# Performance work log

Hardware: AMD Instinct MI355X
Metric: run time of the kernel (lower is better)

The kernel has to match this reference:

```python
import jax, jax.numpy as jnp
import numpy as np

B, S, D = 4, 4096, 1024
H = 16
DH = D // H  # 64, required by the fused kernel


def setup_inputs() -> dict:
    key = jax.random.key(0)
    ks = jax.random.split(key, 5)
    scale = 1.0 / np.sqrt(D)  # xavier-ish init scale for square matrices
    return {
        "x": jax.random.normal(ks[0], (B, S, D), dtype=jnp.float32),
        "Wq": jax.random.normal(ks[1], (D, D), dtype=jnp.float32) * scale,
        "Wk": jax.random.normal(ks[2], (D, D), dtype=jnp.float32) * scale,
        "Wv": jax.random.normal(ks[3], (D, D), dtype=jnp.float32) * scale,
        "Wo": jax.random.normal(ks[4], (D, D), dtype=jnp.float32) * scale,
    }


def reference(x, Wq, Wk, Wv, Wo):
    # Fused QKV projection + linear (non-softmax) attention.
    # Q = x Wq, K = x Wk, V = x Wv, split into H heads of size DH.
    b, s, d = x.shape
    h, dh = H, d // H

    def to_heads(t):
        return t.reshape(b, s, h, dh).transpose(0, 2, 1, 3)  # [B,H,S,dh]

    q = to_heads(jnp.einsum("bsd,de->bse", x, Wq))
    k = to_heads(jnp.einsum("bsd,de->bse", x, Wk))
    v = to_heads(jnp.einsum("bsd,de->bse", x, Wv))

    # Linear attention: O(S * dh^2) per head, never materializes [S,S].
    # out = (1/sqrt(dh)) * Q @ (K^T V)
    scale = 1.0 / jnp.sqrt(jnp.asarray(dh, dtype=x.dtype))
    kv = jnp.einsum("bhsd,bhse->bhde", k, v)          # [B,H,dh,dh]
    out = jnp.einsum("bhsd,bhde->bhse", q, kv) * scale  # [B,H,S,dh]

    # kernel output [B,H,S,dh] -> transpose(1,2) -> view [B,S,D]
    out = out.transpose(0, 2, 1, 3).reshape(b, s, d)
    # out_proj: nn.Linear(D, D, bias=False) -> x @ W.T
    return jnp.einsum("bsd,ed->bse", out, Wo)
```

## Files before the change

### kernel.cpp

```cpp
#include <hip/hip_runtime.h>

typedef unsigned short u16;
typedef unsigned int u32;
typedef u16 u16x8 __attribute__((ext_vector_type(8)));
typedef u16 u16x4 __attribute__((ext_vector_type(4)));
typedef __bf16 bf16x8 __attribute__((ext_vector_type(8)));
typedef float f32x4 __attribute__((ext_vector_type(4)));

__device__ __forceinline__ u16 f2bf(float f) {
    u32 u = __builtin_bit_cast(u32, f);
    u32 r = (u + 0x7fffu + ((u >> 16) & 1u)) >> 16;
    return (u16)r;
}
__device__ __forceinline__ void async16(const u16* g, u16* lds_base) {
    __builtin_amdgcn_global_load_lds(
        (const __attribute__((address_space(1))) void*)g,
        (__attribute__((address_space(3))) void*)lds_base, 16, 0, 0);
}
__device__ __forceinline__ void storeC(float* p, float v) { *p = v; }
__device__ __forceinline__ void storeC(u16* p, float v)   { *p = f2bf(v); }

__global__ void cvt_f32_bf16(const float* __restrict__ in, u16* __restrict__ out, long n) {
    long idx = ((long)blockIdx.x * blockDim.x + threadIdx.x) * 8;
    if (idx >= n) return;
    float4 a = *(const float4*)(in + idx);
    float4 b = *(const float4*)(in + idx + 4);
    u16x8 o;
    o[0] = f2bf(a.x); o[1] = f2bf(a.y); o[2] = f2bf(a.z); o[3] = f2bf(a.w);
    o[4] = f2bf(b.x); o[5] = f2bf(b.y); o[6] = f2bf(b.z); o[7] = f2bf(b.w);
    *(u16x8*)(out + idx) = o;
}

__global__ void transpose_cvt(const float* __restrict__ W0, const float* __restrict__ W1,
                              const float* __restrict__ W2, u16* __restrict__ WT) {
    __shared__ float tile[32][33];
    const float* W = (blockIdx.z == 0) ? W0 : (blockIdx.z == 1) ? W1 : W2;
    int n0 = blockIdx.x * 32, k0 = blockIdx.y * 32;
    int tx = threadIdx.x, ty = threadIdx.y;
#pragma unroll
    for (int r = 0; r < 4; ++r)
        tile[ty + 8 * r][tx] = W[(size_t)(k0 + ty + 8 * r) * 1024 + n0 + tx];
    __syncthreads();
#pragma unroll
    for (int r = 0; r < 4; ++r) {
        int n = n0 + ty + 8 * r;
        WT[((size_t)blockIdx.z * 1024 + n) * 1024 + k0 + tx] = f2bf(tile[tx][ty + 8 * r]);
    }
}

#define BAR __builtin_amdgcn_s_barrier()
#define WAITLGK do { asm volatile("s_waitcnt lgkmcnt(0)" ::: "memory"); \
                     __builtin_amdgcn_sched_barrier(0); } while (0)
#define PRIO1 __builtin_amdgcn_s_setprio(1)
#define PRIO0 __builtin_amdgcn_s_setprio(0)
#define VM(n) asm volatile("s_waitcnt vmcnt(" #n ")" ::: "memory")

#define As SM[0]
#define Bs SM[1]

#define LDA(buf, mh) do { _Pragma("unroll") for (int mi = 0; mi < 4; ++mi) { \
    const int rA = (wm * 128 + (mh) * 64 + mi * 16 + frow) * 64; \
    aF[mi][0] = *(const bf16x8*)&As[buf][rA + xs0]; \
    aF[mi][1] = *(const bf16x8*)&As[buf][rA + xs1]; } } while (0)

#define LDB(buf, nh) do { _Pragma("unroll") for (int ni = 0; ni < 2; ++ni) { \
    const int rB = (wn * 64 + (nh) * 32 + ni * 16 + frow) * 64; \
    bF[(nh) * 2 + ni][0] = *(const bf16x8*)&Bs[buf][rB + xs0]; \
    bF[(nh) * 2 + ni][1] = *(const bf16x8*)&Bs[buf][rB + xs1]; } } while (0)

#define MFQ(mh, nh) do { _Pragma("unroll") for (int mi = 0; mi < 4; ++mi) \
  _Pragma("unroll") for (int ni = 0; ni < 2; ++ni) \
  _Pragma("unroll") for (int s = 0; s < 2; ++s) \
    acc[(mh) * 4 + mi][(nh) * 2 + ni] = __builtin_amdgcn_mfma_f32_16x16x32_bf16( \
        aF[mi][s], bF[(nh) * 2 + ni][s], acc[(mh) * 4 + mi][(nh) * 2 + ni], 0, 0, 0); } while (0)

#define TILE4(buf, S1, S2, S3, S4, WV) \
  LDA(buf, 0); LDB(buf, 0); S1; BAR; WAITLGK; PRIO1; MFQ(0, 0); PRIO0; BAR; \
  LDB(buf, 1); S2; BAR; WAITLGK; PRIO1; MFQ(0, 1); PRIO0; BAR; \
  LDA(buf, 1); S3; BAR; WAITLGK; PRIO1; MFQ(1, 1); PRIO0; BAR; \
  S4; BAR; WAITLGK; PRIO1; MFQ(1, 0); PRIO0; WV; BAR;

template <typename OutT, bool QKV>
__global__ __launch_bounds__(512, 2) void gemm8p(
    const u16* __restrict__ A, int lda,
    const u16* __restrict__ Bt, int ldb,
    OutT* __restrict__ Cq, int ldc, int K, int nTN,
    size_t btStrideB, u16* __restrict__ Kt, u16* __restrict__ Vt) {
    __shared__ u16 SM[2][2][256 * 64];
    const int tid = threadIdx.x;
    const int wid = tid >> 6, lane = tid & 63;
    const int wm = wid >> 2, wn = wid & 3;

    const int nwg = gridDim.x;
    const int orig = blockIdx.x;
    const int id = (orig & 7) * (nwg >> 3) + (orig >> 3);
    const size_t mBase = (size_t)(id / nTN) * 256;
    const size_t nBase = (size_t)(id % nTN) * 256;

    if (!QKV) Bt += (mBase >> 12) * btStrideB;

    const int srow = lane >> 3;
    const int scol = (((lane & 7) ^ (srow & 7)) * 8);

    auto stageH = [&](int buf, int isB, int h, int kt) {
        const u16* g = isB ? Bt : A;
        const int ld = isB ? ldb : lda;
        const size_t rb = isB ? nBase : mBase;
        u16* lds = isB ? Bs[buf] : As[buf];
#pragma unroll
        for (int j = 0; j < 2; ++j) {
            const int rowL = isB ? ((wid >> 1) * 64 + h * 32 + (wid & 1) * 16 + j * 8)
                                 : ((wid >> 2) * 128 + h * 64 + (wid & 3) * 16 + j * 8);
            async16(g + (rb + rowL + srow) * (size_t)ld + (size_t)kt * 64 + scol,
                    lds + rowL * 64);
        }
    };

    const int frow = lane & 15;
    const int xs0 = (((lane >> 4)) ^ (frow & 7)) * 8;
    const int xs1 = ((4 + (lane >> 4)) ^ (frow & 7)) * 8;

    f32x4 acc[8][4] = {};
    bf16x8 aF[4][2], bF[4][2];

#pragma unroll
    for (int h = 0; h < 2; ++h) { stageH(0, 0, h, 0); stageH(0, 1, h, 0); }
#pragma unroll
    for (int h = 0; h < 2; ++h) { stageH(1, 0, h, 1); stageH(1, 1, h, 1); }
    VM(8);
    BAR;

    const int np = K >> 7;
    for (int p = 0; p < np - 1; ++p) {
        const int k2 = 2 * p + 2, k3 = 2 * p + 3;
        TILE4(0, ,
              { stageH(0, 0, 0, k2); stageH(0, 1, 0, k2); },
              stageH(0, 1, 1, k2),
              stageH(0, 0, 1, k2),
              VM(8));
        TILE4(1, ,
              { stageH(1, 0, 0, k3); stageH(1, 1, 0, k3); },
              stageH(1, 1, 1, k3),
              stageH(1, 0, 1, k3),
              VM(8));
    }
    TILE4(0, , , , , VM(0));
    TILE4(1, , , , , );

    const int rb4 = (lane >> 4) * 4;
    const int cx = lane & 15;
    const int sel = QKV ? (int)(nBase >> 10) : 0;
    if (!QKV || sel == 0) {
#pragma unroll
        for (int m = 0; m < 8; ++m) {
#pragma unroll
            for (int n = 0; n < 4; ++n) {
                const size_t col = nBase + wn * 64 + n * 16 + cx;
#pragma unroll
                for (int r = 0; r < 4; ++r) {
                    const size_t row = mBase + wm * 128 + m * 16 + rb4 + r;
                    storeC(&Cq[row * (size_t)ldc + col], acc[m][n][r]);
                }
            }
        }
    } else {
        __syncthreads();
        u16* T = &SM[0][0][0];
        const int nLoc = (int)(nBase & 1023);
#pragma unroll
        for (int n = 0; n < 4; ++n) {
            const int colL = wn * 64 + n * 16 + cx;
#pragma unroll
            for (int m = 0; m < 8; ++m) {
                const int R = wm * 128 + m * 16 + rb4;
                u16x4 v;
                v[0] = f2bf(acc[m][n][0]); v[1] = f2bf(acc[m][n][1]);
                v[2] = f2bf(acc[m][n][2]); v[3] = f2bf(acc[m][n][3]);
                const int byteoff = colL * 512 + ((((R >> 3) ^ (colL & 31)) << 4) | ((R & 7) << 1));
                *(u16x4*)((char*)T + byteoff) = v;
            }
        }
        __syncthreads();
        const int b = (int)(mBase >> 12);
        u16* KV = (sel == 1 ? Kt : Vt);
        const int j = lane & 31;
#pragma unroll
        for (int u = 0; u < 16; ++u) {
            const int iLoc = wid * 32 + u * 2 + (lane >> 5);
            const int byteoff = iLoc * 512 + ((j ^ (iLoc & 31)) << 4);
            const int gcol = nLoc + iLoc;
            u16* dst = KV + (((size_t)(b * 16 + (gcol >> 6)) * 64 + (gcol & 63)) << 12)
                          + (mBase & 4095) + j * 8;
            *(u16x8*)dst = *(const u16x8*)((char*)T + byteoff);
        }
    }
}

__global__ __launch_bounds__(256, 2) void kv_gemm(
    const u16* __restrict__ Kt, const u16* __restrict__ Vt, float* __restrict__ P) {
    __shared__ u16 Ks[64 * 64];
    __shared__ u16 Vs[64 * 64];
    const int chunk = blockIdx.x, bh = blockIdx.y;
    const int tid = threadIdx.x, w = tid >> 6, lane = tid & 63;
    const int srow = lane >> 3;
    const int scol = ((lane & 7) ^ srow) * 8;
    const int frow = lane & 15;
    const int xs0 = ((lane >> 4) ^ (frow & 7)) * 8;
    const int xs1 = ((4 + (lane >> 4)) ^ (frow & 7)) * 8;
    const size_t base = (size_t)bh * 64 * 4096 + (size_t)chunk * 512;
    f32x4 acc[4] = {};
    for (int kk = 0; kk < 8; ++kk) {
        __syncthreads();
#pragma unroll
        for (int j = 0; j < 2; ++j) {
            const int row = w * 16 + j * 8;
            async16(Kt + base + (size_t)(row + srow) * 4096 + kk * 64 + scol, &Ks[row * 64]);
            async16(Vt + base + (size_t)(row + srow) * 4096 + kk * 64 + scol, &Vs[row * 64]);
        }
        asm volatile("s_waitcnt vmcnt(0)" ::: "memory");
        __syncthreads();
        bf16x8 a0 = *(const bf16x8*)&Ks[(w * 16 + frow) * 64 + xs0];
        bf16x8 a1 = *(const bf16x8*)&Ks[(w * 16 + frow) * 64 + xs1];
#pragma unroll
        for (int n = 0; n < 4; ++n) {
            bf16x8 b0 = *(const bf16x8*)&Vs[(n * 16 + frow) * 64 + xs0];
            bf16x8 b1 = *(const bf16x8*)&Vs[(n * 16 + frow) * 64 + xs1];
            acc[n] = __builtin_amdgcn_mfma_f32_16x16x32_bf16(a0, b0, acc[n], 0, 0, 0);
            acc[n] = __builtin_amdgcn_mfma_f32_16x16x32_bf16(a1, b1, acc[n], 0, 0, 0);
        }
    }
    const int rb4 = (lane >> 4) * 4, cx = lane & 15;
    float* p = P + ((size_t)chunk * 64 + bh) * 4096;
#pragma unroll
    for (int n = 0; n < 4; ++n)
#pragma unroll
        for (int r = 0; r < 4; ++r)
            p[(w * 16 + rb4 + r) * 64 + n * 16 + cx] = acc[n][r];
}

__global__ void kv_reduce(const float* __restrict__ P, u16* __restrict__ kvb) {
    const int bh = blockIdx.x, t = threadIdx.x;
    for (int idx = t; idx < 4096; idx += 256) {
        float s = 0.f;
#pragma unroll
        for (int c = 0; c < 8; ++c) s += P[((size_t)c * 64 + bh) * 4096 + idx];
        kvb[(size_t)bh * 4096 + idx] = f2bf(s * 0.125f);
    }
}

__global__ __launch_bounds__(256, 2) void w2_gemm(
    const u16* __restrict__ Wob, const u16* __restrict__ kvb, u16* __restrict__ W2t) {
    __shared__ u16 Aw[256 * 64];
    __shared__ u16 Bw[64 * 64];
    const int eT = blockIdx.x, h = blockIdx.y, b = blockIdx.z;
    const int tid = threadIdx.x, w = tid >> 6, lane = tid & 63;
    const int srow = lane >> 3;
    const int scol = ((lane & 7) ^ srow) * 8;
#pragma unroll
    for (int j = 0; j < 8; ++j) {
        const int row = w * 64 + j * 8;
        async16(Wob + (size_t)(eT * 256 + row + srow) * 1024 + h * 64 + scol, &Aw[row * 64]);
    }
#pragma unroll
    for (int j = 0; j < 2; ++j) {
        const int row = w * 16 + j * 8;
        async16(kvb + ((size_t)(b * 16 + h) * 64 + row + srow) * 64 + scol, &Bw[row * 64]);
    }
    asm volatile("s_waitcnt vmcnt(0)" ::: "memory");
    __syncthreads();
    const int frow = lane & 15;
    const int xs0 = ((lane >> 4) ^ (frow & 7)) * 8;
    const int xs1 = ((4 + (lane >> 4)) ^ (frow & 7)) * 8;
    f32x4 acc[4][4] = {};
#pragma unroll
    for (int m = 0; m < 4; ++m) {
        bf16x8 a0 = *(const bf16x8*)&Aw[(w * 64 + m * 16 + frow) * 64 + xs0];
        bf16x8 a1 = *(const bf16x8*)&Aw[(w * 64 + m * 16 + frow) * 64 + xs1];
#pragma unroll
        for (int n = 0; n < 4; ++n) {
            bf16x8 b0 = *(const bf16x8*)&Bw[(n * 16 + frow) * 64 + xs0];
            bf16x8 b1 = *(const bf16x8*)&Bw[(n * 16 + frow) * 64 + xs1];
            acc[m][n] = __builtin_amdgcn_mfma_f32_16x16x32_bf16(a0, b0, acc[m][n], 0, 0, 0);
            acc[m][n] = __builtin_amdgcn_mfma_f32_16x16x32_bf16(a1, b1, acc[m][n], 0, 0, 0);
        }
    }
    const int rb4 = (lane >> 4) * 4, cx = lane & 15;
    u16* out = W2t + (size_t)b * 1048576;
#pragma unroll
    for (int m = 0; m < 4; ++m)
#pragma unroll
        for (int n = 0; n < 4; ++n)
#pragma unroll
            for (int r = 0; r < 4; ++r)
                out[(size_t)(eT * 256 + w * 64 + m * 16 + rb4 + r) * 1024 + h * 64 + n * 16 + cx] =
                    f2bf(acc[m][n][r]);
}

extern "C" void kernel_launch(void* const* d_in, const int* in_sizes, int n_in,
                              void* d_out, int out_size, void* d_ws, size_t ws_size,
                              hipStream_t stream) {
    const float* x  = (const float*)d_in[0];
    const float* Wq = (const float*)d_in[1];
    const float* Wk = (const float*)d_in[2];
    const float* Wv = (const float*)d_in[3];
    const float* Wo = (const float*)d_in[4];
    float* out = (float*)d_out;
    char* ws = (char*)d_ws;

    u16*   Yq    = (u16*)(ws);
    u16*   Kt    = (u16*)(ws + 33554432);
    u16*   Vt    = (u16*)(ws + 67108864);
    u16*   xb    = (u16*)(ws + 100663296);
    float* Pkv   = (float*)(ws + 100663296);
    u16*   kvb   = (u16*)(ws + 109051904);
    u16*   W2t   = (u16*)(ws + 109576192);
    u16*   WqkvT = (u16*)(ws + 134217728);
    u16*   Wob   = (u16*)(ws + 140509184);

    cvt_f32_bf16<<<8192, 256, 0, stream>>>(x, xb, 16777216L);
    cvt_f32_bf16<<<512, 256, 0, stream>>>(Wo, Wob, 1048576L);
    transpose_cvt<<<dim3(32, 32, 3), dim3(32, 8), 0, stream>>>(Wq, Wk, Wv, WqkvT);

    gemm8p<u16, true><<<768, 512, 0, stream>>>(xb, 1024, WqkvT, 1024, Yq, 1024, 1024, 12,
                                               0, Kt, Vt);

    kv_gemm<<<dim3(8, 64), 256, 0, stream>>>(Kt, Vt, Pkv);
    kv_reduce<<<64, 256, 0, stream>>>(Pkv, kvb);
    w2_gemm<<<dim3(4, 16, 4), 256, 0, stream>>>(Wob, kvb, W2t);

    gemm8p<float, false><<<256, 512, 0, stream>>>(Yq, 1024, W2t, 1024, out, 1024, 1024, 4,
                                                  1048576, nullptr, nullptr);
}
```

Before: 188.2 us.

## Fold Wq into per-batch output weight to skip the Q projection GEMM

```diff
diff --git a/kernel.cpp b/kernel.cpp
--- a/kernel.cpp
+++ b/kernel.cpp
@@ -32,9 +32,9 @@
 }
 
 __global__ void transpose_cvt(const float* __restrict__ W0, const float* __restrict__ W1,
-                              const float* __restrict__ W2, u16* __restrict__ WT) {
+                              u16* __restrict__ WT) {
     __shared__ float tile[32][33];
-    const float* W = (blockIdx.z == 0) ? W0 : (blockIdx.z == 1) ? W1 : W2;
+    const float* W = (blockIdx.z == 0) ? W0 : W1;
     int n0 = blockIdx.x * 32, k0 = blockIdx.y * 32;
     int tx = threadIdx.x, ty = threadIdx.y;
 #pragma unroll
@@ -80,7 +80,7 @@
   LDA(buf, 1); S3; BAR; WAITLGK; PRIO1; MFQ(1, 1); PRIO0; BAR; \
   S4; BAR; WAITLGK; PRIO1; MFQ(1, 0); PRIO0; WV; BAR;
 
-template <typename OutT, bool QKV>
+template <typename OutT, bool KVMODE>
 __global__ __launch_bounds__(512, 2) void gemm8p(
     const u16* __restrict__ A, int lda,
     const u16* __restrict__ Bt, int ldb,
@@ -97,7 +97,7 @@
     const size_t mBase = (size_t)(id / nTN) * 256;
     const size_t nBase = (size_t)(id % nTN) * 256;
 
-    if (!QKV) Bt += (mBase >> 12) * btStrideB;
+    if (!KVMODE) Bt += (mBase >> 12) * btStrideB;
 
     const int srow = lane >> 3;
     const int scol = (((lane & 7) ^ (srow & 7)) * 8);
@@ -149,8 +149,7 @@
 
     const int rb4 = (lane >> 4) * 4;
     const int cx = lane & 15;
-    const int sel = QKV ? (int)(nBase >> 10) : 0;
-    if (!QKV || sel == 0) {
+    if (!KVMODE) {
 #pragma unroll
         for (int m = 0; m < 8; ++m) {
 #pragma unroll
@@ -182,7 +181,7 @@
         }
         __syncthreads();
         const int b = (int)(mBase >> 12);
-        u16* KV = (sel == 1 ? Kt : Vt);
+        u16* KV = ((nBase >> 10) == 0 ? Kt : Vt);
         const int j = lane & 31;
 #pragma unroll
         for (int u = 0; u < 16; ++u) {
@@ -194,6 +193,78 @@
             *(u16x8*)dst = *(const u16x8*)((char*)T + byteoff);
         }
     }
+}
+
+__global__ __launch_bounds__(256, 2) void gemm128(
+    const u16* __restrict__ A, int lda,
+    const u16* __restrict__ Bt, int ldb,
+    u16* __restrict__ C, int ldc, int K) {
+    __shared__ u16 A2[2][128 * 64];
+    __shared__ u16 B2[2][128 * 64];
+    const int tid = threadIdx.x, w = tid >> 6, lane = tid & 63;
+    const int wr = w >> 1, wc = w & 1;
+    const size_t mBase = (size_t)blockIdx.y * 128;
+    const size_t nBase = (size_t)blockIdx.x * 128;
+    const int lr = lane >> 3;
+    const int scol = ((lane & 7) ^ lr) * 8;
+
+    auto stage = [&](int buf, int kt) {
+#pragma unroll
+        for (int c = 0; c < 2; ++c) {
+            const u16* g = c ? Bt : A;
+            const int ld = c ? ldb : lda;
+            const size_t rb = c ? nBase : mBase;
+            u16* lds = c ? B2[buf] : A2[buf];
+#pragma unroll
+            for (int jj = 0; jj < 4; ++jj) {
+                const int rowL = jj * 32 + w * 8;
+                async16(g + (rb + rowL + lr) * (size_t)ld + (size_t)kt * 64 + scol,
+                        lds + rowL * 64);
+            }
+        }
+    };
+
+    const int frow = lane & 15;
+    const int xs0 = ((lane >> 4) ^ (frow & 7)) * 8;
+    const int xs1 = ((4 + (lane >> 4)) ^ (frow & 7)) * 8;
+    f32x4 acc[4][4] = {};
+
+    stage(0, 0);
+    __syncthreads();
+    const int nk = K >> 6;
+    for (int kt = 0; kt < nk; ++kt) {
+        const int cur = kt & 1;
+        if (kt + 1 < nk) stage(cur ^ 1, kt + 1);
+        bf16x8 bF[4][2];
+#pragma unroll
+        for (int n = 0; n < 4; ++n) {
+            const int rB = (wc * 64 + n * 16 + frow) * 64;
+            bF[n][0] = *(const bf16x8*)&B2[cur][rB + xs0];
+            bF[n][1] = *(const bf16x8*)&B2[cur][rB + xs1];
+        }
+#pragma unroll
+        for (int m = 0; m < 4; ++m) {
+            const int rA = (wr * 64 + m * 16 + frow) * 64;
+            bf16x8 a0 = *(const bf16x8*)&A2[cur][rA + xs0];
+            bf16x8 a1 = *(const bf16x8*)&A2[cur][rA + xs1];
+#pragma unroll
+            for (int n = 0; n < 4; ++n) {
+                acc[m][n] = __builtin_amdgcn_mfma_f32_16x16x32_bf16(a0, bF[n][0], acc[m][n], 0, 0, 0);
+                acc[m][n] = __builtin_amdgcn_mfma_f32_16x16x32_bf16(a1, bF[n][1], acc[m][n], 0, 0, 0);
+            }
+        }
+        __syncthreads();
+    }
+    const int rb4 = (lane >> 4) * 4, cx = lane & 15;
+#pragma unroll
+    for (int m = 0; m < 4; ++m)
+#pragma unroll
+        for (int n = 0; n < 4; ++n) {
+            const size_t col = nBase + wc * 64 + n * 16 + cx;
+#pragma unroll
+            for (int r = 0; r < 4; ++r)
+                C[(mBase + wr * 64 + m * 16 + rb4 + r) * (size_t)ldc + col] = f2bf(acc[m][n][r]);
+        }
 }
 
 __global__ __launch_bounds__(256, 2) void kv_gemm(
@@ -307,27 +378,31 @@
     float* out = (float*)d_out;
     char* ws = (char*)d_ws;
 
-    u16*   Yq    = (u16*)(ws);
+    u16*   xb    = (u16*)(ws);
     u16*   Kt    = (u16*)(ws + 33554432);
     u16*   Vt    = (u16*)(ws + 67108864);
-    u16*   xb    = (u16*)(ws + 100663296);
-    float* Pkv   = (float*)(ws + 100663296);
-    u16*   kvb   = (u16*)(ws + 109051904);
-    u16*   W2t   = (u16*)(ws + 109576192);
-    u16*   WqkvT = (u16*)(ws + 134217728);
-    u16*   Wob   = (u16*)(ws + 140509184);
+    u16*   WkvT  = (u16*)(ws + 100663296);
+    u16*   Wqb   = (u16*)(ws + 104857600);
+    u16*   Wob   = (u16*)(ws + 106954752);
+    float* Pkv   = (float*)(ws + 109051904);
+    u16*   kvb   = (u16*)(ws + 117440512);
+    u16*   W2t   = (u16*)(ws + 117964800);
+    u16*   W3T   = (u16*)(ws + 126353408);
 
     cvt_f32_bf16<<<8192, 256, 0, stream>>>(x, xb, 16777216L);
+    cvt_f32_bf16<<<512, 256, 0, stream>>>(Wq, Wqb, 1048576L);
     cvt_f32_bf16<<<512, 256, 0, stream>>>(Wo, Wob, 1048576L);
-    transpose_cvt<<<dim3(32, 32, 3), dim3(32, 8), 0, stream>>>(Wq, Wk, Wv, WqkvT);
-
-    gemm8p<u16, true><<<768, 512, 0, stream>>>(xb, 1024, WqkvT, 1024, Yq, 1024, 1024, 12,
-                                               0, Kt, Vt);
+    transpose_cvt<<<dim3(32, 32, 2), dim3(32, 8), 0, stream>>>(Wk, Wv, WkvT);
+
+    gemm8p<u16, true><<<512, 512, 0, stream>>>(xb, 1024, WkvT, 1024, (u16*)nullptr, 0,
+                                               1024, 8, 0, Kt, Vt);
 
     kv_gemm<<<dim3(8, 64), 256, 0, stream>>>(Kt, Vt, Pkv);
     kv_reduce<<<64, 256, 0, stream>>>(Pkv, kvb);
     w2_gemm<<<dim3(4, 16, 4), 256, 0, stream>>>(Wob, kvb, W2t);
 
-    gemm8p<float, false><<<256, 512, 0, stream>>>(Yq, 1024, W2t, 1024, out, 1024, 1024, 4,
+    gemm128<<<dim3(8, 32), 256, 0, stream>>>(W2t, 1024, Wqb, 1024, W3T, 1024, 1024);
+
+    gemm8p<float, false><<<256, 512, 0, stream>>>(xb, 1024, W3T, 1024, out, 1024, 1024, 4,
                                                   1048576, nullptr, nullptr);
 }
```

Measured after the change: 178.5 us. -5.1%, faster.
